# Kernel tuning notes

Hardware: AMD Instinct MI355X
Metric: run time of the kernel (lower is better)

Reference implementation:

```python
import jax, jax.numpy as jnp
import numpy as np

NUM_SLOTS = 24
EPS = 1e-5

def setup_inputs() -> dict:
    key = jax.random.key(0)
    k1, k2 = jax.random.split(key)
    x = jax.random.normal(k1, (4, 32, 200, 2048), dtype=jnp.float32)
    time = jax.random.randint(k2, (4, 2048), 0, NUM_SLOTS, dtype=jnp.int64)
    return {"x": x, "time": time}

def reference(x, time):
    # x: [b, c, n, t]; time: [b, t] int slot ids in [0, NUM_SLOTS)
    b, c, n, t = x.shape
    time = time[..., -t:]
    idx = time.reshape(b * t)

    # [b*t, n, c] layout matching x.permute(2,0,3,1).reshape(n, b*t, c) contraction
    xf = jnp.transpose(x, (0, 3, 2, 1)).reshape(b * t, n * c)

    # True segment-sum replaces the one-hot matmul; column L1-normalize == divide by slot count
    counts = jax.ops.segment_sum(jnp.ones((b * t,), x.dtype), idx, num_segments=NUM_SLOTS)
    denom = jnp.maximum(counts, 1e-12)[:, None]  # F.normalize eps-clamped norm

    sum_x = jax.ops.segment_sum(xf, idx, num_segments=NUM_SLOTS)            # [S, n*c]
    sum_x2 = jax.ops.segment_sum(xf * xf, idx, num_segments=NUM_SLOTS)      # [S, n*c]

    mean_slot = (sum_x / denom).reshape(NUM_SLOTS, n, c).mean(axis=1)       # [S, c]
    m2_slot = (sum_x2 / denom).reshape(NUM_SLOTS, n, c).mean(axis=1)        # [S, c]
    var_slot = m2_slot - mean_slot ** 2                                     # [S, c]

    # Embedding gather back per (b, t), broadcast over n
    sm = jnp.transpose(mean_slot[time], (0, 2, 1))[:, :, None, :]           # [b, c, 1, t]
    sv = jnp.transpose(var_slot[time], (0, 2, 1))[:, :, None, :]            # [b, c, 1, t]

    return (x - sm) / jnp.sqrt(sv + EPS)
```

## Files before the change

### kernel.cpp

```cpp
#include <hip/hip_runtime.h>
#include <math.h>

#define Bb 4
#define Cc 32
#define Nn 200
#define Tt 2048
#define Ss 24
#define EPSf 1e-5f

typedef float f4 __attribute__((ext_vector_type(4)));
typedef int i4 __attribute__((ext_vector_type(4)));


__global__ __launch_bounds__(256) void k_stats(const float* __restrict__ x,
                                               const int* __restrict__ timei,
                                               float2* __restrict__ part,
                                               int* __restrict__ cntpart) {
    __shared__ float lsum[Ss], lsq[Ss];
    __shared__ int   lcnt[Ss];
    const int tid = threadIdx.x;
    const int bx  = blockIdx.x;
    const int tt = bx & 1;
    const int nc = (bx >> 1) & 7;
    const int bc = bx >> 4;
    const int b  = bc >> 5;
    const int c  = bc & 31;
    const bool do_hist = (c == 0 && nc == 0);

    if (tid < Ss) { lsum[tid] = 0.f; lsq[tid] = 0.f; lcnt[tid] = 0; }
    __syncthreads();

    const int t0 = tt * 1024 + tid * 4;
    const i4 sl = *(const i4*)(timei + b * Tt + t0);

    const size_t plane = ((size_t)(b * Cc + c) * Nn + (size_t)nc * 25) * Tt;
    const float* bp = x + plane + t0;

    float s0 = 0.f, s1 = 0.f, s2 = 0.f, s3 = 0.f;
    float q0 = 0.f, q1 = 0.f, q2 = 0.f, q3 = 0.f;
#pragma unroll 5
    for (int r = 0; r < 25; ++r) {
        f4 v = *(const f4*)(bp + (size_t)r * Tt);
        s0 += v[0]; q0 += v[0] * v[0];
        s1 += v[1]; q1 += v[1] * v[1];
        s2 += v[2]; q2 += v[2] * v[2];
        s3 += v[3]; q3 += v[3] * v[3];
    }

    atomicAdd(&lsum[sl[0]], s0); atomicAdd(&lsq[sl[0]], q0);
    atomicAdd(&lsum[sl[1]], s1); atomicAdd(&lsq[sl[1]], q1);
    atomicAdd(&lsum[sl[2]], s2); atomicAdd(&lsq[sl[2]], q2);
    atomicAdd(&lsum[sl[3]], s3); atomicAdd(&lsq[sl[3]], q3);
    if (do_hist) {
        atomicAdd(&lcnt[sl[0]], 1); atomicAdd(&lcnt[sl[1]], 1);
        atomicAdd(&lcnt[sl[2]], 1); atomicAdd(&lcnt[sl[3]], 1);
    }
    __syncthreads();

    const int chunk = (b * 2 + tt) * 8 + nc;
    if (tid < Ss) {
        part[(c * Ss + tid) * 64 + chunk] = make_float2(lsum[tid], lsq[tid]);
        if (do_hist) cntpart[(b * 2 + tt) * Ss + tid] = lcnt[tid];
    }
}

__global__ __launch_bounds__(256) void k_norm(const float* __restrict__ x,
                                              const int* __restrict__ timei,
                                              const float2* __restrict__ part,
                                              const int* __restrict__ cntpart,
                                              float* __restrict__ out) {
    __shared__ float lsum[Ss], lsq[Ss];
    __shared__ float s_mr[Ss], s_r[Ss];
    const int tid = threadIdx.x;
    const int bx  = blockIdx.x;
    const int b  = bx >> 7;
    const int c  = (bx >> 2) & 31;
    const int nc = bx & 3;

    if (tid < Ss) { lsum[tid] = 0.f; lsq[tid] = 0.f; }
    __syncthreads();
    if (tid < 192) {
        const int s = tid >> 3, j = tid & 7;
        const float2* pp = &part[(c * Ss + s) * 64 + j * 8];
        float ps = 0.f, pq = 0.f;
#pragma unroll
        for (int k = 0; k < 8; ++k) { ps += pp[k].x; pq += pp[k].y; }
        atomicAdd(&lsum[s], ps);
        atomicAdd(&lsq[s],  pq);
    }
    __syncthreads();
    if (tid < Ss) {
        int cnt = 0;
#pragma unroll
        for (int h = 0; h < 8; ++h) cnt += cntpart[h * Ss + tid];
        float denom = fmaxf((float)cnt, 1e-12f) * (float)Nn;
        float m  = lsum[tid] / denom;
        float m2 = lsq[tid]  / denom;
        float rr = 1.0f / sqrtf(m2 - m * m + EPSf);
        s_r[tid]  = rr;
        s_mr[tid] = m * rr;
    }
    __syncthreads();

    const int t0 = tid * 4;
    const i4 sl0 = *(const i4*)(timei + b * Tt + t0);
    const i4 sl1 = *(const i4*)(timei + b * Tt + t0 + 1024);
    const float rr0 = s_r[sl0[0]], mr0 = s_mr[sl0[0]];
    const float rr1 = s_r[sl0[1]], mr1 = s_mr[sl0[1]];
    const float rr2 = s_r[sl0[2]], mr2 = s_mr[sl0[2]];
    const float rr3 = s_r[sl0[3]], mr3 = s_mr[sl0[3]];
    const float rr4 = s_r[sl1[0]], mr4 = s_mr[sl1[0]];
    const float rr5 = s_r[sl1[1]], mr5 = s_mr[sl1[1]];
    const float rr6 = s_r[sl1[2]], mr6 = s_mr[sl1[2]];
    const float rr7 = s_r[sl1[3]], mr7 = s_mr[sl1[3]];

    const size_t plane = ((size_t)(b * Cc + c) * Nn + (size_t)nc * 50) * Tt;
    const float* xp = x + plane + t0;
    float* op = out + plane + t0;

#pragma unroll 5
    for (int r = 0; r < 50; ++r) {
        f4 v0 = *(const f4*)(xp + (size_t)r * Tt);
        f4 v1 = *(const f4*)(xp + (size_t)r * Tt + 1024);
        f4 o0, o1;
        o0[0] = fmaf(v0[0], rr0, -mr0);
        o0[1] = fmaf(v0[1], rr1, -mr1);
        o0[2] = fmaf(v0[2], rr2, -mr2);
        o0[3] = fmaf(v0[3], rr3, -mr3);
        o1[0] = fmaf(v1[0], rr4, -mr4);
        o1[1] = fmaf(v1[1], rr5, -mr5);
        o1[2] = fmaf(v1[2], rr6, -mr6);
        o1[3] = fmaf(v1[3], rr7, -mr7);
        __builtin_nontemporal_store(o0, (f4*)(op + (size_t)r * Tt));
        __builtin_nontemporal_store(o1, (f4*)(op + (size_t)r * Tt + 1024));
    }
}

extern "C" void kernel_launch(void* const* d_in, const int* in_sizes, int n_in,
                              void* d_out, int out_size, void* d_ws, size_t ws_size,
                              hipStream_t stream) {
    const float* x   = (const float*)d_in[0];
    const int* timei = (const int*)d_in[1];
    float* out = (float*)d_out;

    float2* part = (float2*)d_ws;
    int* cnt = (int*)((char*)d_ws + (size_t)Cc * Ss * 64 * sizeof(float2));

    k_stats<<<2048, 256, 0, stream>>>(x, timei, part, cnt);
    k_norm<<<512, 256, 0, stream>>>(x, timei, part, cnt, out);
}
```

Measured before the change: 104.2 us.

## Fuse stats and normalize via grid barrier, caching rows in registers as bf16

Replaces the two-kernel stats-then-normalize scheme with one persistent kernel of 512 blocks. Each block reduces its slab, publishes partial sums, waits at a global atomic-counter barrier, then normalizes. To avoid re-reading x from memory, 40 of its 50 rows are kept in registers, packed as bf16. This cuts HBM traffic but rounds most outputs through bf16, which adds error. It also relies on all 512 blocks being co-resident and on the kernel not spilling registers; a fallback to the old path runs if it spills.

```diff
diff --git a/kernel.cpp b/kernel.cpp
--- a/kernel.cpp
+++ b/kernel.cpp
@@ -7,10 +7,179 @@
 #define Tt 2048
 #define Ss 24
 #define EPSf 1e-5f
+#define GRID 512
+#define RKEEP 40
 
 typedef float f4 __attribute__((ext_vector_type(4)));
 typedef int i4 __attribute__((ext_vector_type(4)));
-
+typedef unsigned u4 __attribute__((ext_vector_type(4)));
+
+__device__ __forceinline__ unsigned rne_bf16(float f) {
+    unsigned u = __float_as_uint(f);
+    return (u + 0x7FFFu + ((u >> 16) & 1u)) >> 16;
+}
+__device__ __forceinline__ unsigned pack2(float a, float b) {
+    return rne_bf16(a) | (rne_bf16(b) << 16);
+}
+__device__ __forceinline__ float lo16(unsigned u) { return __uint_as_float(u << 16); }
+__device__ __forceinline__ float hi16(unsigned u) { return __uint_as_float(u & 0xFFFF0000u); }
+
+
+__global__ void k_zero(int* __restrict__ counter) { *counter = 0; }
+
+#define ROWS40(M) M(0) M(1) M(2) M(3) M(4) M(5) M(6) M(7) M(8) M(9) \
+                  M(10) M(11) M(12) M(13) M(14) M(15) M(16) M(17) M(18) M(19) \
+                  M(20) M(21) M(22) M(23) M(24) M(25) M(26) M(27) M(28) M(29) \
+                  M(30) M(31) M(32) M(33) M(34) M(35) M(36) M(37) M(38) M(39)
+
+#define DROW(i) u4 xb##i;
+
+#define LROW(i) { \
+    f4 v0 = *(const f4*)(bp + (size_t)(i) * Tt); \
+    f4 v1 = *(const f4*)(bp + (size_t)(i) * Tt + 1024); \
+    xb##i[0] = pack2(v0[0], v0[1]); \
+    xb##i[1] = pack2(v0[2], v0[3]); \
+    xb##i[2] = pack2(v1[0], v1[1]); \
+    xb##i[3] = pack2(v1[2], v1[3]); \
+    s0 += v0[0]; q0 += v0[0]*v0[0]; s1 += v0[1]; q1 += v0[1]*v0[1]; \
+    s2 += v0[2]; q2 += v0[2]*v0[2]; s3 += v0[3]; q3 += v0[3]*v0[3]; \
+    s4 += v1[0]; q4 += v1[0]*v1[0]; s5 += v1[1]; q5 += v1[1]*v1[1]; \
+    s6 += v1[2]; q6 += v1[2]*v1[2]; s7 += v1[3]; q7 += v1[3]*v1[3]; }
+
+#define SROW(i) { \
+    f4 o0, o1; \
+    o0[0] = fmaf(lo16(xb##i[0]), rr0, -mr0); \
+    o0[1] = fmaf(hi16(xb##i[0]), rr1, -mr1); \
+    o0[2] = fmaf(lo16(xb##i[1]), rr2, -mr2); \
+    o0[3] = fmaf(hi16(xb##i[1]), rr3, -mr3); \
+    o1[0] = fmaf(lo16(xb##i[2]), rr4, -mr4); \
+    o1[1] = fmaf(hi16(xb##i[2]), rr5, -mr5); \
+    o1[2] = fmaf(lo16(xb##i[3]), rr6, -mr6); \
+    o1[3] = fmaf(hi16(xb##i[3]), rr7, -mr7); \
+    __builtin_nontemporal_store(o0, (f4*)(op + (size_t)(i) * Tt)); \
+    __builtin_nontemporal_store(o1, (f4*)(op + (size_t)(i) * Tt + 1024)); }
+
+__attribute__((amdgpu_waves_per_eu(2, 2)))
+__global__ __launch_bounds__(256) void k_fused(const float* __restrict__ x,
+                                               const int* __restrict__ timei,
+                                               float2* __restrict__ part,
+                                               int* __restrict__ cntp,
+                                               int* __restrict__ counter,
+                                               float* __restrict__ out) {
+    __shared__ float lsum[Ss], lsq[Ss];
+    __shared__ int   lcnt[Ss];
+    __shared__ float s_r[Ss], s_mr[Ss];
+
+    const int tid = threadIdx.x;
+    const int bx  = blockIdx.x;
+    const int b   = bx >> 7;
+    const int c   = (bx >> 2) & 31;
+    const int q   = bx & 3;
+    const bool do_hist = (c == 0 && q == 0);
+
+    if (tid < Ss) { lsum[tid] = 0.f; lsq[tid] = 0.f; lcnt[tid] = 0; }
+    __syncthreads();
+
+    const int t0 = tid * 4;
+    const i4 sl0 = *(const i4*)(timei + b * Tt + t0);
+    const i4 sl1 = *(const i4*)(timei + b * Tt + t0 + 1024);
+
+    const size_t plane = ((size_t)(b * Cc + c) * Nn + (size_t)q * 50) * Tt;
+    const float* bp = x + plane + t0;
+
+    ROWS40(DROW)
+    float s0=0,s1=0,s2=0,s3=0,s4=0,s5=0,s6=0,s7=0;
+    float q0=0,q1=0,q2=0,q3=0,q4=0,q5=0,q6=0,q7=0;
+
+    ROWS40(LROW)
+    for (int r = RKEEP; r < 50; ++r) {
+        f4 v0 = *(const f4*)(bp + (size_t)r * Tt);
+        f4 v1 = *(const f4*)(bp + (size_t)r * Tt + 1024);
+        s0 += v0[0]; q0 += v0[0]*v0[0]; s1 += v0[1]; q1 += v0[1]*v0[1];
+        s2 += v0[2]; q2 += v0[2]*v0[2]; s3 += v0[3]; q3 += v0[3]*v0[3];
+        s4 += v1[0]; q4 += v1[0]*v1[0]; s5 += v1[1]; q5 += v1[1]*v1[1];
+        s6 += v1[2]; q6 += v1[2]*v1[2]; s7 += v1[3]; q7 += v1[3]*v1[3];
+    }
+
+    atomicAdd(&lsum[sl0[0]], s0); atomicAdd(&lsq[sl0[0]], q0);
+    atomicAdd(&lsum[sl0[1]], s1); atomicAdd(&lsq[sl0[1]], q1);
+    atomicAdd(&lsum[sl0[2]], s2); atomicAdd(&lsq[sl0[2]], q2);
+    atomicAdd(&lsum[sl0[3]], s3); atomicAdd(&lsq[sl0[3]], q3);
+    atomicAdd(&lsum[sl1[0]], s4); atomicAdd(&lsq[sl1[0]], q4);
+    atomicAdd(&lsum[sl1[1]], s5); atomicAdd(&lsq[sl1[1]], q5);
+    atomicAdd(&lsum[sl1[2]], s6); atomicAdd(&lsq[sl1[2]], q6);
+    atomicAdd(&lsum[sl1[3]], s7); atomicAdd(&lsq[sl1[3]], q7);
+    if (do_hist) {
+        atomicAdd(&lcnt[sl0[0]], 1); atomicAdd(&lcnt[sl0[1]], 1);
+        atomicAdd(&lcnt[sl0[2]], 1); atomicAdd(&lcnt[sl0[3]], 1);
+        atomicAdd(&lcnt[sl1[0]], 1); atomicAdd(&lcnt[sl1[1]], 1);
+        atomicAdd(&lcnt[sl1[2]], 1); atomicAdd(&lcnt[sl1[3]], 1);
+    }
+    __syncthreads();
+
+    if (tid < Ss) {
+        part[(c * Ss + tid) * 16 + (b * 4 + q)] = make_float2(lsum[tid], lsq[tid]);
+        if (do_hist) cntp[b * Ss + tid] = lcnt[tid];
+    }
+    __syncthreads();
+
+    if (tid == 0) {
+        __threadfence();
+        __hip_atomic_fetch_add(counter, 1, __ATOMIC_ACQ_REL, __HIP_MEMORY_SCOPE_AGENT);
+        while (__hip_atomic_load(counter, __ATOMIC_ACQUIRE, __HIP_MEMORY_SCOPE_AGENT) < GRID)
+            __builtin_amdgcn_s_sleep(2);
+        __threadfence();
+    }
+    __syncthreads();
+
+    if (tid < Ss) { lsum[tid] = 0.f; lsq[tid] = 0.f; }
+    __syncthreads();
+    if (tid < 192) {
+        const int s = tid >> 3, j = tid & 7;
+        float2 p0 = part[(c * Ss + s) * 16 + 2 * j];
+        float2 p1 = part[(c * Ss + s) * 16 + 2 * j + 1];
+        atomicAdd(&lsum[s], p0.x + p1.x);
+        atomicAdd(&lsq[s],  p0.y + p1.y);
+    }
+    __syncthreads();
+    if (tid < Ss) {
+        int cnt = cntp[tid] + cntp[Ss + tid] + cntp[2 * Ss + tid] + cntp[3 * Ss + tid];
+        float denom = fmaxf((float)cnt, 1e-12f) * (float)Nn;
+        float m  = lsum[tid] / denom;
+        float m2 = lsq[tid]  / denom;
+        float rr = 1.0f / sqrtf(m2 - m * m + EPSf);
+        s_r[tid]  = rr;
+        s_mr[tid] = m * rr;
+    }
+    __syncthreads();
+
+    const float rr0 = s_r[sl0[0]], mr0 = s_mr[sl0[0]];
+    const float rr1 = s_r[sl0[1]], mr1 = s_mr[sl0[1]];
+    const float rr2 = s_r[sl0[2]], mr2 = s_mr[sl0[2]];
+    const float rr3 = s_r[sl0[3]], mr3 = s_mr[sl0[3]];
+    const float rr4 = s_r[sl1[0]], mr4 = s_mr[sl1[0]];
+    const float rr5 = s_r[sl1[1]], mr5 = s_mr[sl1[1]];
+    const float rr6 = s_r[sl1[2]], mr6 = s_mr[sl1[2]];
+    const float rr7 = s_r[sl1[3]], mr7 = s_mr[sl1[3]];
+
+    float* op = out + plane + t0;
+    ROWS40(SROW)
+    for (int r = RKEEP; r < 50; ++r) {
+        f4 v0 = *(const f4*)(bp + (size_t)r * Tt);
+        f4 v1 = *(const f4*)(bp + (size_t)r * Tt + 1024);
+        f4 o0, o1;
+        o0[0] = fmaf(v0[0], rr0, -mr0);
+        o0[1] = fmaf(v0[1], rr1, -mr1);
+        o0[2] = fmaf(v0[2], rr2, -mr2);
+        o0[3] = fmaf(v0[3], rr3, -mr3);
+        o1[0] = fmaf(v1[0], rr4, -mr4);
+        o1[1] = fmaf(v1[1], rr5, -mr5);
+        o1[2] = fmaf(v1[2], rr6, -mr6);
+        o1[3] = fmaf(v1[3], rr7, -mr7);
+        __builtin_nontemporal_store(o0, (f4*)(op + (size_t)r * Tt));
+        __builtin_nontemporal_store(o1, (f4*)(op + (size_t)r * Tt + 1024));
+    }
+}
 
 __global__ __launch_bounds__(256) void k_stats(const float* __restrict__ x,
                                                const int* __restrict__ timei,
@@ -143,9 +312,21 @@
     const int* timei = (const int*)d_in[1];
     float* out = (float*)d_out;
 
-    float2* part = (float2*)d_ws;
-    int* cnt = (int*)((char*)d_ws + (size_t)Cc * Ss * 64 * sizeof(float2));
-
-    k_stats<<<2048, 256, 0, stream>>>(x, timei, part, cnt);
-    k_norm<<<512, 256, 0, stream>>>(x, timei, part, cnt, out);
-}
+    hipFuncAttributes fa;
+    bool fused_ok = (hipFuncGetAttributes(&fa, (const void*)k_fused) == hipSuccess)
+                    && fa.localSizeBytes == 0;
+
+    if (fused_ok) {
+        float2* part = (float2*)d_ws;
+        int* cntp    = (int*)((char*)d_ws + (size_t)Cc * Ss * 16 * sizeof(float2));
+        int* counter = (int*)((char*)d_ws + (size_t)Cc * Ss * 16 * sizeof(float2)
+                              + 128 * sizeof(int));
+        k_zero<<<1, 1, 0, stream>>>(counter);
+        k_fused<<<GRID, 256, 0, stream>>>(x, timei, part, cntp, counter, out);
+    } else {
+        float2* part = (float2*)d_ws;
+        int* cnt = (int*)((char*)d_ws + (size_t)Cc * Ss * 64 * sizeof(float2));
+        k_stats<<<2048, 256, 0, stream>>>(x, timei, part, cnt);
+        k_norm<<<512, 256, 0, stream>>>(x, timei, part, cnt, out);
+    }
+}
```

Result: no change. 104.0 us (-0.2%).

## Fuse stats and normalize into one persistent kernel with a grid barrier

Applied to the files above, without the earlier changes.

Merges the statistics and normalization passes into a single kernel of 2048 blocks. After writing its per-slot partials, each block waits at a global atomic-counter barrier, then reduces the partials and normalizes the same tile it just read, hoping the second read hits in cache. The aim is to avoid a full second pass over x from HBM and one kernel launch boundary. It depends on all 2048 blocks being resident at once, which is checked through an occupancy query (at least 8 blocks per CU); otherwise it falls back to the two-kernel path. It adds a zeroing kernel launch and spin-wait time at the barrier.

```diff
diff --git a/kernel.cpp b/kernel.cpp
--- a/kernel.cpp
+++ b/kernel.cpp
@@ -7,10 +7,121 @@
 #define Tt 2048
 #define Ss 24
 #define EPSf 1e-5f
+#define GRIDS 2048
 
 typedef float f4 __attribute__((ext_vector_type(4)));
 typedef int i4 __attribute__((ext_vector_type(4)));
 
+
+__global__ void k_zero(int* __restrict__ counter) { *counter = 0; }
+
+__global__ __launch_bounds__(256) void k_single(const float* __restrict__ x,
+                                                const int* __restrict__ timei,
+                                                float2* __restrict__ part,
+                                                int* __restrict__ cntp,
+                                                int* __restrict__ counter,
+                                                float* __restrict__ out) {
+    __shared__ float lsum[Ss], lsq[Ss];
+    __shared__ int   lcnt[Ss];
+    __shared__ float s_r[Ss], s_mr[Ss];
+
+    const int tid = threadIdx.x;
+    const int bx  = blockIdx.x;
+    const int tt = bx & 1;
+    const int nc = (bx >> 1) & 7;
+    const int bc = bx >> 4;
+    const int b  = bc >> 5;
+    const int c  = bc & 31;
+    const bool do_hist = (c == 0 && nc == 0);
+
+    if (tid < Ss) { lsum[tid] = 0.f; lsq[tid] = 0.f; lcnt[tid] = 0; }
+    __syncthreads();
+
+    const int t0 = tt * 1024 + tid * 4;
+    const i4 sl = *(const i4*)(timei + b * Tt + t0);
+
+    const size_t plane = ((size_t)(b * Cc + c) * Nn + (size_t)nc * 25) * Tt;
+    const float* bp = x + plane + t0;
+
+    float s0 = 0.f, s1 = 0.f, s2 = 0.f, s3 = 0.f;
+    float q0 = 0.f, q1 = 0.f, q2 = 0.f, q3 = 0.f;
+#pragma unroll 5
+    for (int r = 0; r < 25; ++r) {
+        f4 v = *(const f4*)(bp + (size_t)r * Tt);
+        s0 += v[0]; q0 += v[0] * v[0];
+        s1 += v[1]; q1 += v[1] * v[1];
+        s2 += v[2]; q2 += v[2] * v[2];
+        s3 += v[3]; q3 += v[3] * v[3];
+    }
+
+    atomicAdd(&lsum[sl[0]], s0); atomicAdd(&lsq[sl[0]], q0);
+    atomicAdd(&lsum[sl[1]], s1); atomicAdd(&lsq[sl[1]], q1);
+    atomicAdd(&lsum[sl[2]], s2); atomicAdd(&lsq[sl[2]], q2);
+    atomicAdd(&lsum[sl[3]], s3); atomicAdd(&lsq[sl[3]], q3);
+    if (do_hist) {
+        atomicAdd(&lcnt[sl[0]], 1); atomicAdd(&lcnt[sl[1]], 1);
+        atomicAdd(&lcnt[sl[2]], 1); atomicAdd(&lcnt[sl[3]], 1);
+    }
+    __syncthreads();
+
+    const int chunk = (b * 2 + tt) * 8 + nc;
+    if (tid < Ss) {
+        part[(c * Ss + tid) * 64 + chunk] = make_float2(lsum[tid], lsq[tid]);
+        if (do_hist) cntp[(b * 2 + tt) * Ss + tid] = lcnt[tid];
+    }
+    __syncthreads();
+
+    if (tid == 0) {
+        __threadfence();
+        __hip_atomic_fetch_add(counter, 1, __ATOMIC_ACQ_REL, __HIP_MEMORY_SCOPE_AGENT);
+        while (__hip_atomic_load(counter, __ATOMIC_ACQUIRE, __HIP_MEMORY_SCOPE_AGENT) < GRIDS)
+            __builtin_amdgcn_s_sleep(4);
+        __threadfence();
+    }
+    __syncthreads();
+
+    if (tid < Ss) { lsum[tid] = 0.f; lsq[tid] = 0.f; }
+    __syncthreads();
+    if (tid < 192) {
+        const int s = tid >> 3, j = tid & 7;
+        const float2* pp = &part[(c * Ss + s) * 64 + j * 8];
+        float ps = 0.f, pq = 0.f;
+#pragma unroll
+        for (int k = 0; k < 8; ++k) { ps += pp[k].x; pq += pp[k].y; }
+        atomicAdd(&lsum[s], ps);
+        atomicAdd(&lsq[s],  pq);
+    }
+    __syncthreads();
+    if (tid < Ss) {
+        int cnt = 0;
+#pragma unroll
+        for (int h = 0; h < 8; ++h) cnt += cntp[h * Ss + tid];
+        float denom = fmaxf((float)cnt, 1e-12f) * (float)Nn;
+        float m  = lsum[tid] / denom;
+        float m2 = lsq[tid]  / denom;
+        float rr = 1.0f / sqrtf(m2 - m * m + EPSf);
+        s_r[tid]  = rr;
+        s_mr[tid] = m * rr;
+    }
+    __syncthreads();
+
+    const float rr0 = s_r[sl[0]], mr0 = s_mr[sl[0]];
+    const float rr1 = s_r[sl[1]], mr1 = s_mr[sl[1]];
+    const float rr2 = s_r[sl[2]], mr2 = s_mr[sl[2]];
+    const float rr3 = s_r[sl[3]], mr3 = s_mr[sl[3]];
+
+    float* op = out + plane + t0;
+#pragma unroll 5
+    for (int r = 0; r < 25; ++r) {
+        f4 v = *(const f4*)(bp + (size_t)r * Tt);
+        f4 o;
+        o[0] = fmaf(v[0], rr0, -mr0);
+        o[1] = fmaf(v[1], rr1, -mr1);
+        o[2] = fmaf(v[2], rr2, -mr2);
+        o[3] = fmaf(v[3], rr3, -mr3);
+        __builtin_nontemporal_store(o, (f4*)(op + (size_t)r * Tt));
+    }
+}
 
 __global__ __launch_bounds__(256) void k_stats(const float* __restrict__ x,
                                                const int* __restrict__ timei,
@@ -144,8 +255,23 @@
     float* out = (float*)d_out;
 
     float2* part = (float2*)d_ws;
-    int* cnt = (int*)((char*)d_ws + (size_t)Cc * Ss * 64 * sizeof(float2));
-
-    k_stats<<<2048, 256, 0, stream>>>(x, timei, part, cnt);
-    k_norm<<<512, 256, 0, stream>>>(x, timei, part, cnt, out);
-}
+    int* cntp    = (int*)((char*)d_ws + (size_t)Cc * Ss * 64 * sizeof(float2));
+    int* counter = cntp + 8 * Ss + 128;
+
+    hipFuncAttributes fa;
+    bool fused_ok = (hipFuncGetAttributes(&fa, (const void*)k_single) == hipSuccess)
+                    && fa.localSizeBytes == 0;
+    if (fused_ok) {
+        int occ = 0;
+        fused_ok = (hipOccupancyMaxActiveBlocksPerMultiprocessor(&occ, k_single, 256, 0)
+                    == hipSuccess) && occ >= 8;
+    }
+
+    if (fused_ok) {
+        k_zero<<<1, 1, 0, stream>>>(counter);
+        k_single<<<GRIDS, 256, 0, stream>>>(x, timei, part, cntp, counter, out);
+    } else {
+        k_stats<<<2048, 256, 0, stream>>>(x, timei, part, cntp);
+        k_norm<<<512, 256, 0, stream>>>(x, timei, part, cntp, out);
+    }
+}
```

Measured after the change: 103.8 us. Within noise of the previous version (-0.4%).
